# Kernel tuning notes

Measured on AMD Instinct MI355X. Metric: run time of the kernel, lower is better.

The kernel has to match this reference:

```python
import jax, jax.numpy as jnp
import numpy as np

B, T, C, H = 4, 2048, 1024, 16
D = C // H

def setup_inputs() -> dict:
    key = jax.random.key(0)
    k1, k2, k3, k4 = jax.random.split(key, 4)
    s = 1.0 / np.sqrt(C)
    return {
        "x": jax.random.normal(k1, (B, T, C), dtype=jnp.float32),
        "W_qkv": jax.random.normal(k2, (3 * C, C), dtype=jnp.float32) * s,
        "W_out": jax.random.normal(k3, (C, C), dtype=jnp.float32) * s,
        "b_out": jax.random.normal(k4, (C,), dtype=jnp.float32) * s,
    }

def reference(x, W_qkv, W_out, b_out):
    Bx, Tx, Cx = x.shape
    # qkv projection (torch Linear: y = x @ W.T), bias=False
    qkv = x @ W_qkv.T                               # [B,T,3C]
    q, k, v = jnp.split(qkv, 3, axis=-1)
    def heads(t):
        return t.reshape(Bx, Tx, H, D).transpose(0, 2, 1, 3)  # [B,H,T,D]
    q, k, v = heads(q), heads(k), heads(v)
    scale = 1.0 / jnp.sqrt(jnp.asarray(D, dtype=x.dtype))
    scores = jnp.einsum("bhqd,bhkd->bhqk", q, k) * scale      # [B,H,T,T]
    causal = jnp.tril(jnp.ones((Tx, Tx), dtype=bool))
    scores = jnp.where(causal[None, None], scores, -jnp.inf)
    attn = jax.nn.softmax(scores, axis=-1)                    # dropout p=0 (eval)
    out = jnp.einsum("bhqk,bhkd->bhqd", attn, v)              # [B,H,T,D]
    out = out.transpose(0, 2, 1, 3).reshape(Bx, Tx, Cx)       # [B,T,C]
    return out @ W_out.T + b_out
```

## Files before the change

### kernel.cpp

```cpp
#include <hip/hip_runtime.h>


typedef __attribute__((ext_vector_type(8))) __bf16 bf16x8;
typedef __attribute__((ext_vector_type(4))) float f32x4;
typedef __attribute__((ext_vector_type(16))) float f32x16;

__device__ __forceinline__ unsigned short f2bf(float f) {
  union { float f; unsigned u; } v; v.f = f;
  unsigned r = v.u + 0x7fffu + ((v.u >> 16) & 1u);
  return (unsigned short)(r >> 16);
}

__device__ __forceinline__ unsigned cvtpk(float lo, float hi) {
  unsigned r;
  asm("v_cvt_pk_bf16_f32 %0, %1, %2" : "=v"(r) : "v"(lo), "v"(hi));
  return r;
}

__device__ __forceinline__ float fexp2(float x) {
  float r;
  asm("v_exp_f32 %0, %1" : "=v"(r) : "v"(x));
  return r;
}
__device__ __forceinline__ float max3f(float a, float b, float c) {
  return fmaxf(fmaxf(a, b), c);
}

__device__ __forceinline__ void gld16(const void* g, void* l) {
  __builtin_amdgcn_global_load_lds(
      (const __attribute__((address_space(1))) void*)g,
      (__attribute__((address_space(3))) void*)l, 16, 0, 0);
}

__device__ __forceinline__ f32x4 mfma16(bf16x8 a, bf16x8 b, f32x4 c) {
  return __builtin_amdgcn_mfma_f32_16x16x32_bf16(a, b, c, 0, 0, 0);
}
__device__ __forceinline__ f32x16 mfma32(bf16x8 a, bf16x8 b, f32x16 c) {
  return __builtin_amdgcn_mfma_f32_32x32x16_bf16(a, b, c, 0, 0, 0);
}

__global__ __launch_bounds__(256) void cast_f32_bf16(
    const float* __restrict__ src, unsigned short* __restrict__ dst, int n) {
  int i = (blockIdx.x * 256 + threadIdx.x) * 4;
  if (i >= n) return;
  float4 v = *(const float4*)(src + i);
  ushort4 o;
  o.x = f2bf(v.x); o.y = f2bf(v.y); o.z = f2bf(v.z); o.w = f2bf(v.w);
  *(ushort4*)(dst + i) = o;
}

__device__ __forceinline__ bf16x8 ldsw128(const char* mat, int row, int cb) {
  return *(const bf16x8*)(mat + row * 128 + (cb ^ ((row & 7) << 4)));
}

#define PH_SYNC_A() do { __builtin_amdgcn_s_barrier();              \
    asm volatile("s_waitcnt lgkmcnt(0)" ::: "memory");              \
    __builtin_amdgcn_sched_barrier(0); } while (0)
#define PH_SYNC_B() do { __builtin_amdgcn_s_barrier();              \
    __builtin_amdgcn_sched_barrier(0); } while (0)
#define VMC6() asm volatile("s_waitcnt vmcnt(6)" ::: "memory")
#define VMC2() asm volatile("s_waitcnt vmcnt(2)" ::: "memory")
#define VMC0() asm volatile("s_waitcnt vmcnt(0)" ::: "memory")

__device__ __forceinline__ void stage_half(const char* gbase, char* mat,
                                           int kt, int half, int tid) {
#pragma unroll
  for (int q = 0; q < 2; ++q) {
    const int r = half * 128 + q * 64 + (tid >> 3);
    const int cb = (tid & 7) * 16;
    gld16(gbase + (size_t)r * 2048 + kt * 128 + (cb ^ ((r & 7) << 4)),
          mat + r * 128 + cb);
  }
}
__device__ __forceinline__ void stage_A(const char* gbase, char* mat,
                                        int kt, int tid) {
#pragma unroll
  for (int q = 0; q < 2; ++q) {
    const int r = q * 64 + (tid >> 3);
    const int cb = (tid & 7) * 16;
    gld16(gbase + (size_t)r * 2048 + kt * 128 + (cb ^ ((r & 7) << 4)),
          mat + r * 128 + cb);
  }
}

template <int MODE>
__global__ __launch_bounds__(512, 2) void gemm2p(
    const unsigned short* __restrict__ A, const unsigned short* __restrict__ Bm,
    unsigned short* __restrict__ qo, unsigned short* __restrict__ ko,
    unsigned short* __restrict__ vo,
    const float* __restrict__ bias, float* __restrict__ fout) {
  __shared__ char lds[98304];
  const int tid = threadIdx.x;
  const int w = tid >> 6, l = tid & 63, lr = l & 15, lg = l >> 4;
  const int wm = w >> 2, wn = w & 3;
  constexpr int GX = (MODE == 0) ? 12 : 4;
  constexpr int NWG = GX * 64;
  const int L = blockIdx.x + blockIdx.y * GX;
  const int logical = (L & 7) * (NWG >> 3) + (L >> 3);
  const int m0 = (logical / GX) * 128, n0 = (logical % GX) * 256;
  const char* Ag = (const char*)A + (size_t)m0 * 2048;
  const char* Bg = (const char*)Bm + (size_t)n0 * 2048;
  char* A0 = lds;            char* A1 = lds + 16384;
  char* B0 = lds + 32768;    char* B1 = lds + 65536;

  f32x4 acc[4][4];
  f32x4 zero = {0.f, 0.f, 0.f, 0.f};
#pragma unroll
  for (int i = 0; i < 4; i++)
#pragma unroll
    for (int jj = 0; jj < 4; jj++) acc[i][jj] = zero;

  stage_A(Ag, A0, 0, tid);
  stage_half(Bg, B0, 0, 0, tid);
  stage_half(Bg, B0, 0, 1, tid);
  stage_A(Ag, A1, 1, tid);
  stage_half(Bg, B1, 1, 0, tid);
  stage_half(Bg, B1, 1, 1, tid);
  VMC6();
  __builtin_amdgcn_s_barrier();
  __builtin_amdgcn_sched_barrier(0);

  for (int t = 0; t < 16; ++t) {
    char* As = (t & 1) ? A1 : A0;
    char* Bs = (t & 1) ? B1 : B0;
    char* Bo = (t & 1) ? B0 : B1;
    bf16x8 aF[4][2], bF[2][2];

#pragma unroll
    for (int mq = 0; mq < 4; ++mq) {
      const int row = (mq >> 1) * 64 + wm * 32 + (mq & 1) * 16 + lr;
#pragma unroll
      for (int kk = 0; kk < 2; ++kk)
        aF[mq][kk] = ldsw128(As, row, kk * 64 + lg * 16);
    }
#pragma unroll
    for (int nt = 0; nt < 2; ++nt) {
      const int row = wn * 64 + nt * 16 + lr;
#pragma unroll
      for (int kk = 0; kk < 2; ++kk)
        bF[nt][kk] = ldsw128(Bs, row, kk * 64 + lg * 16);
    }
    if (t >= 1 && t < 15) {
      stage_half(Bg, Bo, t + 1, 0, tid);
      stage_half(Bg, Bo, t + 1, 1, tid);
    }
    PH_SYNC_A();
    __builtin_amdgcn_s_setprio(1);
#pragma unroll
    for (int mq = 0; mq < 4; ++mq)
#pragma unroll
      for (int nt = 0; nt < 2; ++nt)
#pragma unroll
        for (int kk = 0; kk < 2; ++kk)
          acc[mq][nt] = mfma16(aF[mq][kk], bF[nt][kk], acc[mq][nt]);
    __builtin_amdgcn_s_setprio(0);
    PH_SYNC_B();

#pragma unroll
    for (int nt = 0; nt < 2; ++nt) {
      const int row = wn * 64 + (2 + nt) * 16 + lr;
#pragma unroll
      for (int kk = 0; kk < 2; ++kk)
        bF[nt][kk] = ldsw128(Bs, row, kk * 64 + lg * 16);
    }
    if (t < 14) stage_A(Ag, As, t + 2, tid);
    PH_SYNC_A();
    __builtin_amdgcn_s_setprio(1);
#pragma unroll
    for (int mq = 0; mq < 4; ++mq)
#pragma unroll
      for (int nt = 0; nt < 2; ++nt)
#pragma unroll
        for (int kk = 0; kk < 2; ++kk)
          acc[mq][2 + nt] = mfma16(aF[mq][kk], bF[nt][kk], acc[mq][2 + nt]);
    __builtin_amdgcn_s_setprio(0);
    if (t < 14) VMC2(); else if (t < 15) VMC0();
    PH_SYNC_B();
  }

  if (MODE == 1) {
#pragma unroll
    for (int mq = 0; mq < 4; ++mq) {
#pragma unroll
      for (int nt = 0; nt < 4; ++nt) {
        int n = n0 + wn * 64 + nt * 16 + lr;
        int mb = m0 + (mq >> 1) * 64 + wm * 32 + (mq & 1) * 16 + lg * 4;
        float bv = bias[n];
#pragma unroll
        for (int i = 0; i < 4; i++)
          fout[(size_t)(mb + i) * 1024 + n] = acc[mq][nt][i] + bv;
      }
    }
    return;
  }

  const int ty = n0 >> 10;
  const int hbase = (n0 & 1023) >> 6;
  const int bb = m0 >> 11;
  const int tloc = m0 & 2047;

  if (ty < 2) {
    unsigned short* dst = (ty == 0) ? qo : ko;
    const float sc = (ty == 0) ? 0.18033688011111687f : 1.0f;
    const int h = hbase + wn;
#pragma unroll
    for (int mq = 0; mq < 4; ++mq) {
#pragma unroll
      for (int nt = 0; nt < 4; ++nt) {
        const int dd = nt * 16 + lr;
        const int trow = tloc + (mq >> 1) * 64 + wm * 32 + (mq & 1) * 16 + lg * 4;
#pragma unroll
        for (int i = 0; i < 4; i++)
          dst[((size_t)(bb * 16 + h) * 2048 + trow + i) * 64 + dd] =
              f2bf(acc[mq][nt][i] * sc);
      }
    }
  } else {
#pragma unroll
    for (int mq = 0; mq < 4; ++mq) {
      const int mcb = ((mq >> 1) * 64 + wm * 32 + (mq & 1) * 16 + lg * 4) * 2;
#pragma unroll
      for (int nt = 0; nt < 4; ++nt) {
        const int row = wn * 64 + nt * 16 + lr;
        uint2 pk;
        pk.x = cvtpk(acc[mq][nt][0], acc[mq][nt][1]);
        pk.y = cvtpk(acc[mq][nt][2], acc[mq][nt][3]);
        *(uint2*)(lds + row * 256 + (mcb ^ ((row & 15) << 4))) = pk;
      }
    }
    __builtin_amdgcn_s_barrier();
    const int hi = tid >> 7, r = tid & 127;
    const int dd = r & 63, seg = r >> 6;
    const int nrow = hi * 64 + dd;
    unsigned short* gp = vo +
        ((size_t)(bb * 16 + hbase + hi) * 64 + dd) * 2048 + tloc + seg * 64;
#pragma unroll
    for (int j = 0; j < 8; ++j) {
      uint4 vd = *(const uint4*)(lds + nrow * 256 +
                                 ((seg * 128 + j * 16) ^ ((nrow & 15) << 4)));
      *(uint4*)(gp + j * 8) = vd;
    }
  }
}

__device__ __forceinline__ bf16x8 ldsw(const char* base, int row, int cb) {
  return *(const bf16x8*)(base + row * 128 + (cb ^ ((row & 7) << 4)));
}

__global__ __launch_bounds__(512, 4) void attn_causal(
    const unsigned short* __restrict__ qg, const unsigned short* __restrict__ kg,
    const unsigned short* __restrict__ vtg, unsigned short* __restrict__ og) {
  __shared__ char lds[32768];
  const int tid = threadIdx.x;
  const int w = tid >> 6, l = tid & 63, lo = l & 31, hi = l >> 5;
  const int bh = blockIdx.x;
  const int qc = (0x31204657u >> (blockIdx.y * 4)) & 7;
  const int q0 = qc * 256;
  const int nkv = qc * 4 + 4;
  const int b = bh >> 4, h = bh & 15;
  const char* kpB = (const char*)(kg + (size_t)bh * 131072);
  const char* vpB = (const char*)(vtg + (size_t)bh * 131072);
  const unsigned short* qp = qg + (size_t)bh * 131072;
  const int qrow = q0 + 8 * lo + w;

  bf16x8 qf[4];
#pragma unroll
  for (int c = 0; c < 4; ++c)
    qf[c] = *(const bf16x8*)(qp + (size_t)qrow * 64 + hi * 8 + c * 16);

  f32x16 ov[2];
#pragma unroll
  for (int r = 0; r < 16; ++r) { ov[0][r] = 0.f; ov[1][r] = 0.f; }
  const f32x16 zz = {0.f, 0.f, 0.f, 0.f, 0.f, 0.f, 0.f, 0.f,
                     0.f, 0.f, 0.f, 0.f, 0.f, 0.f, 0.f, 0.f};
  float m = -__builtin_inff(), lsum = 0.f;

  const int srow = tid >> 3;
  const int scb = ((tid & 7) * 16) ^ ((srow & 7) << 4);

  gld16(kpB + (size_t)srow * 128 + scb, lds + tid * 16);
  gld16(vpB + (size_t)srow * 4096 + scb, lds + 8192 + tid * 16);
  __syncthreads();

  for (int kt = 0; kt < nkv; ++kt) {
    const int k0 = kt * 64;
    if (kt + 1 < nkv) {
      char* nb = lds + ((kt + 1) & 1) * 16384;
      gld16(kpB + (size_t)(k0 + 64 + srow) * 128 + scb, nb + tid * 16);
      gld16(vpB + (size_t)srow * 4096 + (size_t)(k0 + 64) * 2 + scb, nb + 8192 + tid * 16);
    }
    const char* Kbuf = lds + (kt & 1) * 16384;
    const char* Vbuf = Kbuf + 8192;

    f32x16 sv[2];
    __builtin_amdgcn_s_setprio(1);
#pragma unroll
    for (int c = 0; c < 4; ++c) {
      bf16x8 kf0 = ldsw(Kbuf, lo, hi * 16 + c * 32);
      bf16x8 kf1 = ldsw(Kbuf, 32 + lo, hi * 16 + c * 32);
      if (c == 0) {
        sv[0] = mfma32(kf0, qf[0], zz);
        sv[1] = mfma32(kf1, qf[0], zz);
      } else {
        sv[0] = mfma32(kf0, qf[c], sv[0]);
        sv[1] = mfma32(kf1, qf[c], sv[1]);
      }
    }
    __builtin_amdgcn_s_setprio(0);

    if (kt >= nkv - 4) {
#pragma unroll
      for (int t = 0; t < 2; ++t)
#pragma unroll
        for (int r = 0; r < 16; ++r) {
          int kgl = k0 + t * 32 + (r & 3) + 8 * (r >> 2) + 4 * hi;
          if (kgl > qrow) sv[t][r] = -__builtin_inff();
        }
    }

    float t0m = max3f(sv[0][0], sv[0][1], sv[0][2]);
    float t1m = max3f(sv[0][3], sv[0][4], sv[0][5]);
    float t2m = max3f(sv[0][6], sv[0][7], sv[0][8]);
    float t3m = max3f(sv[0][9], sv[0][10], sv[0][11]);
    float t4m = max3f(sv[0][12], sv[0][13], sv[0][14]);
    float t5m = max3f(sv[0][15], sv[1][0], sv[1][1]);
    float t6m = max3f(sv[1][2], sv[1][3], sv[1][4]);
    float t7m = max3f(sv[1][5], sv[1][6], sv[1][7]);
    float t8m = max3f(sv[1][8], sv[1][9], sv[1][10]);
    float t9m = max3f(sv[1][11], sv[1][12], sv[1][13]);
    float tam = fmaxf(sv[1][14], sv[1][15]);
    float u0 = max3f(t0m, t1m, t2m);
    float u1 = max3f(t3m, t4m, t5m);
    float u2 = max3f(t6m, t7m, t8m);
    float u3 = fmaxf(t9m, tam);
    float tm = fmaxf(max3f(u0, u1, u2), u3);
    tm = fmaxf(tm, __shfl_xor(tm, 32, 64));

    if (!__all(tm <= m + 8.f)) {
      float nm = fmaxf(fmaxf(m, tm), -1e30f);
      float f = fexp2(m - nm);
      m = nm;
      lsum *= f;
#pragma unroll
      for (int r = 0; r < 16; ++r) { ov[0][r] *= f; ov[1][r] *= f; }
    }

    float ps0 = 0.f, ps1 = 0.f, ps2 = 0.f, ps3 = 0.f;
#pragma unroll
    for (int t = 0; t < 2; ++t)
#pragma unroll
      for (int r = 0; r < 16; r += 4) {
        float p0 = fexp2(sv[t][r + 0] - m);
        float p1 = fexp2(sv[t][r + 1] - m);
        float p2 = fexp2(sv[t][r + 2] - m);
        float p3 = fexp2(sv[t][r + 3] - m);
        sv[t][r + 0] = p0; sv[t][r + 1] = p1;
        sv[t][r + 2] = p2; sv[t][r + 3] = p3;
        ps0 += p0; ps1 += p1; ps2 += p2; ps3 += p3;
      }
    lsum += (ps0 + ps1) + (ps2 + ps3);

    __builtin_amdgcn_s_setprio(1);
#pragma unroll
    for (int c = 0; c < 4; ++c) {
      const int t = c >> 1, rb = (c & 1) * 8;
      unsigned wA = cvtpk(sv[t][rb + 0], sv[t][rb + 1]);
      unsigned wB = cvtpk(sv[t][rb + 2], sv[t][rb + 3]);
      unsigned wC = cvtpk(sv[t][rb + 4], sv[t][rb + 5]);
      unsigned wD = cvtpk(sv[t][rb + 6], sv[t][rb + 7]);
      asm volatile("v_permlane32_swap_b32 %0, %1" : "+v"(wA), "+v"(wC));
      asm volatile("v_permlane32_swap_b32 %0, %1" : "+v"(wB), "+v"(wD));
      union { uint4 u; bf16x8 h; } pc;
      pc.u.x = wA; pc.u.y = wB; pc.u.z = wC; pc.u.w = wD;
      bf16x8 vf0 = ldsw(Vbuf, lo, hi * 16 + c * 32);
      bf16x8 vf1 = ldsw(Vbuf, 32 + lo, hi * 16 + c * 32);
      ov[0] = mfma32(vf0, pc.h, ov[0]);
      ov[1] = mfma32(vf1, pc.h, ov[1]);
    }
    __builtin_amdgcn_s_setprio(0);
    __syncthreads();
  }

  float lt = lsum + __shfl_xor(lsum, 32, 64);
  float inv = 1.0f / lt;
  char* outl = lds + w * 4096;
#pragma unroll
  for (int t2 = 0; t2 < 2; ++t2)
#pragma unroll
    for (int rp = 0; rp < 8; ++rp) {
      const int r = rp * 2;
      const int d0 = (r & 3) + 8 * (r >> 2) + 4 * hi + 32 * t2;
      unsigned pw = cvtpk(ov[t2][r] * inv, ov[t2][r + 1] * inv);
      *(unsigned*)(outl + lo * 128 + ((d0 * 2) ^ ((lo & 7) << 4))) = pw;
    }
  __syncthreads();
  {
    const int qi = l >> 1, cbb = (l & 1) * 64;
    const int t = q0 + 8 * qi + w;
    unsigned short* gp = og + ((size_t)(b * 2048 + t)) * 1024 + h * 64 + (cbb >> 1);
#pragma unroll
    for (int i = 0; i < 4; ++i) {
      uint4 vdat = *(const uint4*)(outl + qi * 128 + ((cbb + i * 16) ^ ((qi & 7) << 4)));
      *(uint4*)(gp + i * 8) = vdat;
    }
  }
}

extern "C" void kernel_launch(void* const* d_in, const int* in_sizes, int n_in,
                              void* d_out, int out_size, void* d_ws, size_t ws_size,
                              hipStream_t stream) {
  const float* x = (const float*)d_in[0];
  const float* Wqkv = (const float*)d_in[1];
  const float* Wout = (const float*)d_in[2];
  const float* bout = (const float*)d_in[3];
  float* out = (float*)d_out;
  char* ws = (char*)d_ws;

  unsigned short* xb = (unsigned short*)(ws);
  unsigned short* wqb = (unsigned short*)(ws + 16777216);
  unsigned short* wob = (unsigned short*)(ws + 23068672);
  unsigned short* qb = (unsigned short*)(ws + 25165824);
  unsigned short* kb = (unsigned short*)(ws + 41943040);
  unsigned short* vtb = (unsigned short*)(ws + 58720256);
  unsigned short* ogb = xb;

  cast_f32_bf16<<<8192, 256, 0, stream>>>(x, xb, 8388608);
  cast_f32_bf16<<<3072, 256, 0, stream>>>(Wqkv, wqb, 3145728);
  cast_f32_bf16<<<1024, 256, 0, stream>>>(Wout, wob, 1048576);

  gemm2p<0><<<dim3(12, 64), 512, 0, stream>>>(xb, wqb, qb, kb, vtb, nullptr, nullptr);
  attn_causal<<<dim3(64, 8), 512, 0, stream>>>(qb, kb, vtb, ogb);
  gemm2p<1><<<dim3(4, 64), 512, 0, stream>>>(ogb, wob, nullptr, nullptr, nullptr, bout, out);
}
```

Before: 158.2 us.

## Load GEMM B operand directly from global, halve LDS, merge cast kernels

```diff
diff --git a/kernel.cpp b/kernel.cpp
--- a/kernel.cpp
+++ b/kernel.cpp
@@ -39,14 +39,21 @@
   return __builtin_amdgcn_mfma_f32_32x32x16_bf16(a, b, c, 0, 0, 0);
 }
 
-__global__ __launch_bounds__(256) void cast_f32_bf16(
-    const float* __restrict__ src, unsigned short* __restrict__ dst, int n) {
+__global__ __launch_bounds__(256) void cast_all(
+    const float* __restrict__ x, const float* __restrict__ wq,
+    const float* __restrict__ wo, unsigned short* __restrict__ xb,
+    unsigned short* __restrict__ wqb, unsigned short* __restrict__ wob) {
   int i = (blockIdx.x * 256 + threadIdx.x) * 4;
-  if (i >= n) return;
-  float4 v = *(const float4*)(src + i);
+  const float* s;
+  unsigned short* d;
+  int off;
+  if (i < 8388608) { s = x; d = xb; off = i; }
+  else if (i < 11534336) { s = wq; d = wqb; off = i - 8388608; }
+  else { s = wo; d = wob; off = i - 11534336; }
+  float4 v = *(const float4*)(s + off);
   ushort4 o;
   o.x = f2bf(v.x); o.y = f2bf(v.y); o.z = f2bf(v.z); o.w = f2bf(v.w);
-  *(ushort4*)(dst + i) = o;
+  *(ushort4*)(d + off) = o;
 }
 
 __device__ __forceinline__ bf16x8 ldsw128(const char* mat, int row, int cb) {
@@ -58,20 +65,9 @@
     __builtin_amdgcn_sched_barrier(0); } while (0)
 #define PH_SYNC_B() do { __builtin_amdgcn_s_barrier();              \
     __builtin_amdgcn_sched_barrier(0); } while (0)
-#define VMC6() asm volatile("s_waitcnt vmcnt(6)" ::: "memory")
 #define VMC2() asm volatile("s_waitcnt vmcnt(2)" ::: "memory")
 #define VMC0() asm volatile("s_waitcnt vmcnt(0)" ::: "memory")
 
-__device__ __forceinline__ void stage_half(const char* gbase, char* mat,
-                                           int kt, int half, int tid) {
-#pragma unroll
-  for (int q = 0; q < 2; ++q) {
-    const int r = half * 128 + q * 64 + (tid >> 3);
-    const int cb = (tid & 7) * 16;
-    gld16(gbase + (size_t)r * 2048 + kt * 128 + (cb ^ ((r & 7) << 4)),
-          mat + r * 128 + cb);
-  }
-}
 __device__ __forceinline__ void stage_A(const char* gbase, char* mat,
                                         int kt, int tid) {
 #pragma unroll
@@ -84,12 +80,12 @@
 }
 
 template <int MODE>
-__global__ __launch_bounds__(512, 2) void gemm2p(
+__global__ __launch_bounds__(512, 4) void gemm2p(
     const unsigned short* __restrict__ A, const unsigned short* __restrict__ Bm,
     unsigned short* __restrict__ qo, unsigned short* __restrict__ ko,
     unsigned short* __restrict__ vo,
     const float* __restrict__ bias, float* __restrict__ fout) {
-  __shared__ char lds[98304];
+  __shared__ char lds[65536];
   const int tid = threadIdx.x;
   const int w = tid >> 6, l = tid & 63, lr = l & 15, lg = l >> 4;
   const int wm = w >> 2, wn = w & 3;
@@ -100,8 +96,8 @@
   const int m0 = (logical / GX) * 128, n0 = (logical % GX) * 256;
   const char* Ag = (const char*)A + (size_t)m0 * 2048;
   const char* Bg = (const char*)Bm + (size_t)n0 * 2048;
-  char* A0 = lds;            char* A1 = lds + 16384;
-  char* B0 = lds + 32768;    char* B1 = lds + 65536;
+  char* A0 = lds;
+  char* A1 = lds + 16384;
 
   f32x4 acc[4][4];
   f32x4 zero = {0.f, 0.f, 0.f, 0.f};
@@ -111,38 +107,29 @@
     for (int jj = 0; jj < 4; jj++) acc[i][jj] = zero;
 
   stage_A(Ag, A0, 0, tid);
-  stage_half(Bg, B0, 0, 0, tid);
-  stage_half(Bg, B0, 0, 1, tid);
   stage_A(Ag, A1, 1, tid);
-  stage_half(Bg, B1, 1, 0, tid);
-  stage_half(Bg, B1, 1, 1, tid);
-  VMC6();
+  VMC2();
   __builtin_amdgcn_s_barrier();
   __builtin_amdgcn_sched_barrier(0);
 
   for (int t = 0; t < 16; ++t) {
     char* As = (t & 1) ? A1 : A0;
-    char* Bs = (t & 1) ? B1 : B0;
-    char* Bo = (t & 1) ? B0 : B1;
     bf16x8 aF[4][2], bF[2][2];
 
+#pragma unroll
+    for (int nt = 0; nt < 2; ++nt) {
+      const int row = wn * 64 + nt * 16 + lr;
+#pragma unroll
+      for (int kk = 0; kk < 2; ++kk)
+        bF[nt][kk] = *(const bf16x8*)(Bg + (size_t)row * 2048 + t * 128 +
+                                      kk * 64 + lg * 16);
+    }
 #pragma unroll
     for (int mq = 0; mq < 4; ++mq) {
       const int row = (mq >> 1) * 64 + wm * 32 + (mq & 1) * 16 + lr;
 #pragma unroll
       for (int kk = 0; kk < 2; ++kk)
         aF[mq][kk] = ldsw128(As, row, kk * 64 + lg * 16);
-    }
-#pragma unroll
-    for (int nt = 0; nt < 2; ++nt) {
-      const int row = wn * 64 + nt * 16 + lr;
-#pragma unroll
-      for (int kk = 0; kk < 2; ++kk)
-        bF[nt][kk] = ldsw128(Bs, row, kk * 64 + lg * 16);
-    }
-    if (t >= 1 && t < 15) {
-      stage_half(Bg, Bo, t + 1, 0, tid);
-      stage_half(Bg, Bo, t + 1, 1, tid);
     }
     PH_SYNC_A();
     __builtin_amdgcn_s_setprio(1);
@@ -161,7 +148,8 @@
       const int row = wn * 64 + (2 + nt) * 16 + lr;
 #pragma unroll
       for (int kk = 0; kk < 2; ++kk)
-        bF[nt][kk] = ldsw128(Bs, row, kk * 64 + lg * 16);
+        bF[nt][kk] = *(const bf16x8*)(Bg + (size_t)row * 2048 + t * 128 +
+                                      kk * 64 + lg * 16);
     }
     if (t < 14) stage_A(Ag, As, t + 2, tid);
     PH_SYNC_A();
@@ -424,9 +412,7 @@
   unsigned short* vtb = (unsigned short*)(ws + 58720256);
   unsigned short* ogb = xb;
 
-  cast_f32_bf16<<<8192, 256, 0, stream>>>(x, xb, 8388608);
-  cast_f32_bf16<<<3072, 256, 0, stream>>>(Wqkv, wqb, 3145728);
-  cast_f32_bf16<<<1024, 256, 0, stream>>>(Wout, wob, 1048576);
+  cast_all<<<12288, 256, 0, stream>>>(x, Wqkv, Wout, xb, wqb, wob);
 
   gemm2p<0><<<dim3(12, 64), 512, 0, stream>>>(xb, wqb, qb, kb, vtb, nullptr, nullptr);
   attn_causal<<<dim3(64, 8), 512, 0, stream>>>(qb, kb, vtb, ogb);
```

Result: slower. 272.6 us (+72.3%).
